# Kernel optimization log

Hardware: AMD Instinct MI355X
Metric: run time of the kernel (lower is better)

Reference implementation:

```python
import jax, jax.numpy as jnp
import numpy as np

N_NODES = 100000
N_EDGES = 3200000
N_FEAT = 64
HID = 64
GDIM = 32
N_CLASS = 2
NUM_GRAPHS = 16


def setup_inputs() -> dict:
    key = jax.random.key(0)
    ks = jax.random.split(key, 24)

    def w(k, fan_in, fan_out):
        return (jax.random.normal(k, (fan_in, fan_out), jnp.float32) / np.sqrt(fan_in)).astype(jnp.float32)

    inp = {
        'x': jax.random.normal(ks[0], (N_NODES, N_FEAT), jnp.float32),
        'edge_index': jax.random.randint(ks[1], (2, N_EDGES), 0, N_NODES, jnp.int32),
        'batch': jnp.sort(jax.random.randint(ks[2], (N_NODES,), 0, NUM_GRAPHS, jnp.int32)),
        # lin0: nr_features -> nhid0
        'lin0_w': w(ks[3], N_FEAT, HID), 'lin0_b': jnp.zeros((HID,), jnp.float32),
        # SAGEConv 1: lin_l (aggregated, with bias), lin_r (self, no bias)
        's1_lw': w(ks[4], HID, HID), 's1_lb': jnp.zeros((HID,), jnp.float32), 's1_rw': w(ks[5], HID, HID),
        # SAGEConv 2
        's2_lw': w(ks[6], HID, HID), 's2_lb': jnp.zeros((HID,), jnp.float32), 's2_rw': w(ks[7], HID, HID),
        # embedding heads
        'emb0_w': w(ks[8], HID, GDIM), 'emb0_b': jnp.zeros((GDIM,), jnp.float32),
        'emb1_w': w(ks[9], HID, GDIM), 'emb1_b': jnp.zeros((GDIM,), jnp.float32),
        'emb2_w': w(ks[10], HID, GDIM), 'emb2_b': jnp.zeros((GDIM,), jnp.float32),
        'merge_w': w(ks[11], 3 * GDIM, GDIM), 'merge_b': jnp.zeros((GDIM,), jnp.float32),
        # global attention pooling: gate_nn (GDIM->1), v_nn (GDIM->GDIM)
        'gate_w': w(ks[12], GDIM, 1), 'gate_b': jnp.zeros((1,), jnp.float32),
        'v_w': w(ks[13], GDIM, GDIM), 'v_b': jnp.zeros((GDIM,), jnp.float32),
        'out_w': w(ks[14], GDIM, N_CLASS), 'out_b': jnp.zeros((N_CLASS,), jnp.float32),
    }
    return inp


def _sage(x, src, dst, lw, lb, rw):
    # mean aggregation of source features at destination nodes
    deg = jax.ops.segment_sum(jnp.ones_like(src, jnp.float32), dst, num_segments=N_NODES)
    agg = jax.ops.segment_sum(x[src], dst, num_segments=N_NODES)
    mean = agg / jnp.maximum(deg, 1.0)[:, None]
    return mean @ lw + lb + x @ rw


def reference(x, edge_index, batch,
              lin0_w, lin0_b, s1_lw, s1_lb, s1_rw, s2_lw, s2_lb, s2_rw,
              emb0_w, emb0_b, emb1_w, emb1_b, emb2_w, emb2_b,
              merge_w, merge_b, gate_w, gate_b, v_w, v_b, out_w, out_b):
    src, dst = edge_index[0], edge_index[1]
    x0 = x @ lin0_w + lin0_b                       # [N, HID]
    x1 = _sage(x0, src, dst, s1_lw, s1_lb, s1_rw)  # [N, HID]
    x2 = _sage(x1, src, dst, s2_lw, s2_lb, s2_rw)  # [N, HID]
    # eval mode: dropout = identity
    e0 = jax.nn.relu(x0 @ emb0_w + emb0_b)
    e1 = jax.nn.relu(x1 @ emb1_w + emb1_b)
    e2 = jax.nn.relu(x2 @ emb2_w + emb2_b)
    xc = jax.nn.relu(jnp.concatenate([e0, e1, e2], axis=1) @ merge_w + merge_b)  # [N, GDIM]
    # global attention pooling with per-graph softmax
    g = (xc @ gate_w + gate_b)[:, 0]               # [N]
    v = xc @ v_w + v_b                             # [N, GDIM]
    m = jax.ops.segment_max(g, batch, num_segments=NUM_GRAPHS)
    e = jnp.exp(g - m[batch])
    d = jax.ops.segment_sum(e, batch, num_segments=NUM_GRAPHS)
    a = e / d[batch]
    pooled = jax.ops.segment_sum(a[:, None] * v, batch, num_segments=NUM_GRAPHS)  # [NG, GDIM]
    logits = pooled @ out_w + out_b                # [NG, 2]
    output1 = jax.nn.softmax(logits, axis=-1)
    output2 = logits
    return (output1, output2)
```

## Files before the change

### kernel.cpp

```cpp
#include <hip/hip_runtime.h>
#include <hip/hip_bf16.h>
#include <hip/hip_fp16.h>

#define N_NODES 100000
#define N_EDGES 3200000
#define HID 64
#define GDIM 32
#define NUM_GRAPHS 16
#define NB1 256
#define BSHIFT 9
#define B1 512

__device__ __forceinline__ unsigned fkey(float f) {
    unsigned u = __float_as_uint(f);
    return (u & 0x80000000u) ? ~u : (u | 0x80000000u);
}
__device__ __forceinline__ float funkey(unsigned k) {
    unsigned u = (k & 0x80000000u) ? (k ^ 0x80000000u) : ~k;
    return __uint_as_float(u);
}

struct half4 { __half2 lo, hi; };

__global__ __launch_bounds__(256) void hist1_kernel(const int* __restrict__ dst, int* __restrict__ h1, int E4) {
    __shared__ int h[NB1];
    int t = threadIdx.x, b = blockIdx.x;
    h[t] = 0;
    __syncthreads();
    for (int i = b * 256 + t; i < E4; i += B1 * 256) {
        int4 d = ((const int4*)dst)[i];
        atomicAdd(&h[d.x >> BSHIFT], 1);
        atomicAdd(&h[d.y >> BSHIFT], 1);
        atomicAdd(&h[d.z >> BSHIFT], 1);
        atomicAdd(&h[d.w >> BSHIFT], 1);
    }
    __syncthreads();
    h1[b * NB1 + t] = h[t];
}

__global__ __launch_bounds__(256) void scan1_kernel(const int* __restrict__ h1, int* __restrict__ off1,
                                                    int* __restrict__ bstart, int E) {
    __shared__ int ts[256];
    int t = threadIdx.x;
    int tot = 0;
    for (int k = 0; k < B1; k++) tot += h1[k * NB1 + t];
    ts[t] = tot;
    __syncthreads();
    for (int off = 1; off < 256; off <<= 1) {
        int v = (t >= off) ? ts[t - off] : 0;
        __syncthreads();
        ts[t] += v;
        __syncthreads();
    }
    int base = ts[t] - tot;
    bstart[t] = base;
    if (t == 255) bstart[256] = E;
    int run = base;
    for (int k = 0; k < B1; k++) { off1[k * NB1 + t] = run; run += h1[k * NB1 + t]; }
}

__global__ __launch_bounds__(256) void scatter1_kernel(const int* __restrict__ src, const int* __restrict__ dst,
                                                       const int* __restrict__ off1, int* __restrict__ pairs, int E4) {
    __shared__ int cur[NB1];
    int t = threadIdx.x, b = blockIdx.x;
    cur[t] = off1[b * NB1 + t];
    __syncthreads();
    for (int i = b * 256 + t; i < E4; i += B1 * 256) {
        int4 d = ((const int4*)dst)[i];
        int4 s = ((const int4*)src)[i];
        int p0 = atomicAdd(&cur[d.x >> BSHIFT], 1);
        int p1 = atomicAdd(&cur[d.y >> BSHIFT], 1);
        int p2 = atomicAdd(&cur[d.z >> BSHIFT], 1);
        int p3 = atomicAdd(&cur[d.w >> BSHIFT], 1);
        pairs[p0] = (s.x << BSHIFT) | (d.x & 511);
        pairs[p1] = (s.y << BSHIFT) | (d.y & 511);
        pairs[p2] = (s.z << BSHIFT) | (d.z & 511);
        pairs[p3] = (s.w << BSHIFT) | (d.w & 511);
    }
}

__global__ __launch_bounds__(256) void bucket_csr_kernel(const int* __restrict__ pairs, const int* __restrict__ bstart,
                                                         int* __restrict__ rowstart, int* __restrict__ csr,
                                                         int N, int E) {
    __shared__ int hist[512];
    __shared__ int ts[256];
    int b = blockIdx.x, t = threadIdx.x;
    int estart = bstart[b], eend = bstart[b + 1];
    hist[t] = 0; hist[t + 256] = 0;
    __syncthreads();
    for (int e = estart + t; e < eend; e += 256) {
        int pr = pairs[e];
        atomicAdd(&hist[pr & 511], 1);
    }
    __syncthreads();
    int a0 = hist[2 * t], a1 = hist[2 * t + 1];
    int s = a0 + a1;
    ts[t] = s;
    __syncthreads();
    for (int off = 1; off < 256; off <<= 1) {
        int v = (t >= off) ? ts[t - off] : 0;
        __syncthreads();
        ts[t] += v;
        __syncthreads();
    }
    int excl = ts[t] - s;
    __syncthreads();
    hist[2 * t]     = estart + excl;
    hist[2 * t + 1] = estart + excl + a0;
    int nb0 = b << BSHIFT;
    int i0 = nb0 + 2 * t, i1 = i0 + 1;
    if (i0 < N) rowstart[i0] = estart + excl;
    if (i1 < N) rowstart[i1] = estart + excl + a0;
    if (b == gridDim.x - 1 && t == 0) rowstart[N] = E;
    __syncthreads();
    for (int e = estart + t; e < eend; e += 256) {
        int pr = pairs[e];
        int p = atomicAdd(&hist[pr & 511], 1);
        csr[p] = pr >> BSHIFT;
    }
}

__global__ __launch_bounds__(256) void lin0_kernel(const float* __restrict__ x, const float* __restrict__ W,
                            const float* __restrict__ b, float* __restrict__ y, __half* __restrict__ yh, int N) {
    __shared__ __align__(16) float Wl[64 * 64];
    __shared__ float bl[64];
    int t = threadIdx.x;
    for (int i = t; i < 64 * 64; i += 256) Wl[i] = W[i];
    if (t < 64) bl[t] = b[t];
    __syncthreads();
    int row = blockIdx.x * 256 + t;
    if (row >= N) return;
    float acc[64];
#pragma unroll
    for (int j = 0; j < 64; j++) acc[j] = bl[j];
    const float4* xr = (const float4*)(x + (size_t)row * 64);
#pragma unroll
    for (int c = 0; c < 16; c++) {
        float4 xv = xr[c];
        float xs[4] = {xv.x, xv.y, xv.z, xv.w};
#pragma unroll
        for (int kk = 0; kk < 4; kk++) {
            int k = c * 4 + kk;
#pragma unroll
            for (int j4 = 0; j4 < 16; j4++) {
                float4 w = *(const float4*)&Wl[k * 64 + j4 * 4];
                acc[j4 * 4 + 0] += xs[kk] * w.x;
                acc[j4 * 4 + 1] += xs[kk] * w.y;
                acc[j4 * 4 + 2] += xs[kk] * w.z;
                acc[j4 * 4 + 3] += xs[kk] * w.w;
            }
        }
    }
    float4* yr = (float4*)(y + (size_t)row * 64);
#pragma unroll
    for (int c = 0; c < 16; c++)
        yr[c] = make_float4(acc[c * 4], acc[c * 4 + 1], acc[c * 4 + 2], acc[c * 4 + 3]);
    __half2* hr = (__half2*)(yh + (size_t)row * 64);
#pragma unroll
    for (int c = 0; c < 32; c++)
        hr[c] = __halves2half2(__float2half_rn(acc[c * 2]), __float2half_rn(acc[c * 2 + 1]));
}

__global__ __launch_bounds__(256) void agg_kernel(const __half* __restrict__ xh, const int* __restrict__ rowstart,
                           const int* __restrict__ csr, float* __restrict__ meanout, int N) {
    int wid = threadIdx.x >> 6, lane = threadIdx.x & 63;
    int node = blockIdx.x * 4 + wid;
    if (node >= N) return;
    int ro = rowstart[node], re = rowstart[node + 1];
    int g = lane >> 4, c4 = lane & 15;
    float4 acc = make_float4(0.f, 0.f, 0.f, 0.f);
    for (int base = ro; base < re; base += 64) {
        int rem = re - base;
        int idx = 0;
        if (lane < rem) idx = csr[base + lane];
        int kmax = rem < 64 ? rem : 64;
        for (int k = 0; k < kmax; k += 4) {
            int e = k + g;
            int s = __shfl(idx, e);
            if (e < kmax) {
                half4 hv = *(const half4*)(xh + (size_t)s * 64 + (c4 << 2));
                float2 f0 = __half22float2(hv.lo);
                float2 f1 = __half22float2(hv.hi);
                acc.x += f0.x; acc.y += f0.y; acc.z += f1.x; acc.w += f1.y;
            }
        }
    }
#pragma unroll
    for (int off = 16; off < 64; off <<= 1) {
        acc.x += __shfl_xor(acc.x, off);
        acc.y += __shfl_xor(acc.y, off);
        acc.z += __shfl_xor(acc.z, off);
        acc.w += __shfl_xor(acc.w, off);
    }
    int deg = re - ro;
    float inv = 1.0f / (float)(deg > 0 ? deg : 1);
    if (lane < 16) {
        ((float4*)(meanout + (size_t)node * 64))[c4] =
            make_float4(acc.x * inv, acc.y * inv, acc.z * inv, acc.w * inv);
    }
}

__global__ __launch_bounds__(256) void sage_kernel(const float* __restrict__ mean, const float* __restrict__ xin,
                            const float* __restrict__ lw, const float* __restrict__ lb,
                            const float* __restrict__ rw, float* __restrict__ xout,
                            __half* __restrict__ xhout, int N) {
    __shared__ __align__(16) float LW[64 * 64];
    __shared__ __align__(16) float RW[64 * 64];
    __shared__ float LB[64];
    int t = threadIdx.x;
    for (int i = t; i < 64 * 64; i += 256) { LW[i] = lw[i]; RW[i] = rw[i]; }
    if (t < 64) LB[t] = lb[t];
    __syncthreads();
    int row = blockIdx.x * 256 + t;
    if (row >= N) return;
    float acc[64];
#pragma unroll
    for (int j = 0; j < 64; j++) acc[j] = LB[j];
    const float4* mr = (const float4*)(mean + (size_t)row * 64);
    const float4* xr = (const float4*)(xin + (size_t)row * 64);
#pragma unroll
    for (int c = 0; c < 16; c++) {
        float4 xv = mr[c];
        float xs[4] = {xv.x, xv.y, xv.z, xv.w};
#pragma unroll
        for (int kk = 0; kk < 4; kk++) {
            int k = c * 4 + kk;
#pragma unroll
            for (int j4 = 0; j4 < 16; j4++) {
                float4 w = *(const float4*)&LW[k * 64 + j4 * 4];
                acc[j4 * 4 + 0] += xs[kk] * w.x;
                acc[j4 * 4 + 1] += xs[kk] * w.y;
                acc[j4 * 4 + 2] += xs[kk] * w.z;
                acc[j4 * 4 + 3] += xs[kk] * w.w;
            }
        }
    }
#pragma unroll
    for (int c = 0; c < 16; c++) {
        float4 xv = xr[c];
        float xs[4] = {xv.x, xv.y, xv.z, xv.w};
#pragma unroll
        for (int kk = 0; kk < 4; kk++) {
            int k = c * 4 + kk;
#pragma unroll
            for (int j4 = 0; j4 < 16; j4++) {
                float4 w = *(const float4*)&RW[k * 64 + j4 * 4];
                acc[j4 * 4 + 0] += xs[kk] * w.x;
                acc[j4 * 4 + 1] += xs[kk] * w.y;
                acc[j4 * 4 + 2] += xs[kk] * w.z;
                acc[j4 * 4 + 3] += xs[kk] * w.w;
            }
        }
    }
    float4* yr = (float4*)(xout + (size_t)row * 64);
#pragma unroll
    for (int c = 0; c < 16; c++)
        yr[c] = make_float4(acc[c * 4], acc[c * 4 + 1], acc[c * 4 + 2], acc[c * 4 + 3]);
    if (xhout) {
        __half2* hr = (__half2*)(xhout + (size_t)row * 64);
#pragma unroll
        for (int c = 0; c < 32; c++)
            hr[c] = __halves2half2(__float2half_rn(acc[c * 2]), __float2half_rn(acc[c * 2 + 1]));
    }
}

__global__ __launch_bounds__(256) void head_kernel(const float* __restrict__ x0, const float* __restrict__ x1,
                            const float* __restrict__ x2, const int* __restrict__ batch,
                            const float* __restrict__ e0w, const float* __restrict__ e0b,
                            const float* __restrict__ e1w, const float* __restrict__ e1b,
                            const float* __restrict__ e2w, const float* __restrict__ e2b,
                            const float* __restrict__ mw, const float* __restrict__ mb,
                            const float* __restrict__ gw, const float* __restrict__ gbp,
                            const float* __restrict__ vw, const float* __restrict__ vb,
                            float* __restrict__ gout, float* __restrict__ vout,
                            unsigned* __restrict__ mkey, int N) {
    __shared__ __align__(16) __half EW[3 * 2048];
    __shared__ __align__(16) __half MW[96 * 32];
    __shared__ __align__(16) __half VW[32 * 32];
    __shared__ float EB[96], MB[32], GW[32], VB[32];
    __shared__ float GB;
    __shared__ unsigned smax[16];
    int t = threadIdx.x;
    for (int i = t; i < 2048; i += 256) {
        EW[i]        = __float2half_rn(e0w[i]);
        EW[2048 + i] = __float2half_rn(e1w[i]);
        EW[4096 + i] = __float2half_rn(e2w[i]);
    }
    for (int i = t; i < 3072; i += 256) MW[i] = __float2half_rn(mw[i]);
    for (int i = t; i < 1024; i += 256) VW[i] = __float2half_rn(vw[i]);
    if (t < 32) { EB[t] = e0b[t]; EB[32 + t] = e1b[t]; EB[64 + t] = e2b[t];
                  MB[t] = mb[t]; GW[t] = gw[t]; VB[t] = vb[t]; }
    if (t == 0) GB = gbp[0];
    if (t < 16) smax[t] = 0u;
    __syncthreads();
    int node = blockIdx.x * 256 + t;
    if (node < N) {
        float xc[32];
#pragma unroll
        for (int j = 0; j < 32; j++) xc[j] = MB[j];
        const float* px[3] = {x0 + (size_t)node * 64, x1 + (size_t)node * 64, x2 + (size_t)node * 64};
        for (int h = 0; h < 3; h++) {
            float e[32];
#pragma unroll
            for (int j = 0; j < 32; j++) e[j] = EB[h * 32 + j];
            const float4* xr = (const float4*)px[h];
#pragma unroll
            for (int c = 0; c < 16; c++) {
                float4 xv = xr[c];
                float xs[4] = {xv.x, xv.y, xv.z, xv.w};
#pragma unroll
                for (int kk = 0; kk < 4; kk++) {
                    int k = c * 4 + kk;
#pragma unroll
                    for (int j4 = 0; j4 < 8; j4++) {
                        half4 hw = *(const half4*)&EW[h * 2048 + k * 32 + j4 * 4];
                        float2 w0 = __half22float2(hw.lo);
                        float2 w1 = __half22float2(hw.hi);
                        e[j4 * 4 + 0] += xs[kk] * w0.x;
                        e[j4 * 4 + 1] += xs[kk] * w0.y;
                        e[j4 * 4 + 2] += xs[kk] * w1.x;
                        e[j4 * 4 + 3] += xs[kk] * w1.y;
                    }
                }
            }
#pragma unroll
            for (int j = 0; j < 32; j++) e[j] = fmaxf(e[j], 0.f);
#pragma unroll
            for (int i = 0; i < 32; i++) {
#pragma unroll
                for (int j4 = 0; j4 < 8; j4++) {
                    half4 hw = *(const half4*)&MW[(h * 32 + i) * 32 + j4 * 4];
                    float2 w0 = __half22float2(hw.lo);
                    float2 w1 = __half22float2(hw.hi);
                    xc[j4 * 4 + 0] += e[i] * w0.x;
                    xc[j4 * 4 + 1] += e[i] * w0.y;
                    xc[j4 * 4 + 2] += e[i] * w1.x;
                    xc[j4 * 4 + 3] += e[i] * w1.y;
                }
            }
        }
#pragma unroll
        for (int j = 0; j < 32; j++) xc[j] = fmaxf(xc[j], 0.f);
        float g = GB;
#pragma unroll
        for (int i = 0; i < 32; i++) g += xc[i] * GW[i];
        float vv[32];
#pragma unroll
        for (int j = 0; j < 32; j++) vv[j] = VB[j];
#pragma unroll
        for (int i = 0; i < 32; i++) {
#pragma unroll
            for (int j4 = 0; j4 < 8; j4++) {
                half4 hw = *(const half4*)&VW[i * 32 + j4 * 4];
                float2 w0 = __half22float2(hw.lo);
                float2 w1 = __half22float2(hw.hi);
                vv[j4 * 4 + 0] += xc[i] * w0.x;
                vv[j4 * 4 + 1] += xc[i] * w0.y;
                vv[j4 * 4 + 2] += xc[i] * w1.x;
                vv[j4 * 4 + 3] += xc[i] * w1.y;
            }
        }
        gout[node] = g;
        float4* vr = (float4*)(vout + (size_t)node * 32);
#pragma unroll
        for (int c = 0; c < 8; c++)
            vr[c] = make_float4(vv[c * 4], vv[c * 4 + 1], vv[c * 4 + 2], vv[c * 4 + 3]);
        atomicMax(&smax[batch[node]], fkey(g));
    }
    __syncthreads();
    if (t < 16) atomicMax(&mkey[t], smax[t]);
}

__global__ __launch_bounds__(256) void pool_kernel(const float* __restrict__ g, const float* __restrict__ v,
                            const int* __restrict__ batch, const unsigned* __restrict__ mkey,
                            float* __restrict__ dsum, float* __restrict__ pooled, int N) {
    __shared__ float sd[16];
    __shared__ float sp[16 * 32];
    __shared__ float sm[16];
    int t = threadIdx.x;
    if (t < 16) { sd[t] = 0.f; sm[t] = funkey(mkey[t]); }
    for (int i = t; i < 512; i += 256) sp[i] = 0.f;
    __syncthreads();
    int node = blockIdx.x * 256 + t;
    if (node < N) {
        int b = batch[node];
        float e = __expf(g[node] - sm[b]);
        atomicAdd(&sd[b], e);
        const float4* vr = (const float4*)(v + (size_t)node * 32);
#pragma unroll
        for (int c = 0; c < 8; c++) {
            float4 vv = vr[c];
            atomicAdd(&sp[b * 32 + c * 4 + 0], e * vv.x);
            atomicAdd(&sp[b * 32 + c * 4 + 1], e * vv.y);
            atomicAdd(&sp[b * 32 + c * 4 + 2], e * vv.z);
            atomicAdd(&sp[b * 32 + c * 4 + 3], e * vv.w);
        }
    }
    __syncthreads();
    if (t < 16) atomicAdd(&dsum[t], sd[t]);
    for (int i = t; i < 512; i += 256) atomicAdd(&pooled[i], sp[i]);
}

__global__ __launch_bounds__(64) void final_kernel(const float* __restrict__ dsum, const float* __restrict__ pooled,
                             const float* __restrict__ ow, const float* __restrict__ ob,
                             float* __restrict__ out) {
    int t = threadIdx.x;
    if (t >= 16) return;
    float d = dsum[t];
    float l0 = ob[0], l1 = ob[1];
    for (int i = 0; i < 32; i++) {
        float p = pooled[t * 32 + i] / d;
        l0 += p * ow[i * 2 + 0];
        l1 += p * ow[i * 2 + 1];
    }
    float m = fmaxf(l0, l1);
    float e0 = __expf(l0 - m), e1 = __expf(l1 - m);
    float s = e0 + e1;
    out[t * 2 + 0] = e0 / s;
    out[t * 2 + 1] = e1 / s;
    out[32 + t * 2 + 0] = l0;
    out[32 + t * 2 + 1] = l1;
}

extern "C" void kernel_launch(void* const* d_in, const int* in_sizes, int n_in,
                              void* d_out, int out_size, void* d_ws, size_t ws_size,
                              hipStream_t stream) {
    const float* x       = (const float*)d_in[0];
    const int*   ei      = (const int*)d_in[1];
    const int*   batch   = (const int*)d_in[2];
    const float* lin0_w  = (const float*)d_in[3];
    const float* lin0_b  = (const float*)d_in[4];
    const float* s1_lw   = (const float*)d_in[5];
    const float* s1_lb   = (const float*)d_in[6];
    const float* s1_rw   = (const float*)d_in[7];
    const float* s2_lw   = (const float*)d_in[8];
    const float* s2_lb   = (const float*)d_in[9];
    const float* s2_rw   = (const float*)d_in[10];
    const float* e0w     = (const float*)d_in[11];
    const float* e0b     = (const float*)d_in[12];
    const float* e1w     = (const float*)d_in[13];
    const float* e1b     = (const float*)d_in[14];
    const float* e2w     = (const float*)d_in[15];
    const float* e2b     = (const float*)d_in[16];
    const float* mw      = (const float*)d_in[17];
    const float* mb      = (const float*)d_in[18];
    const float* gw      = (const float*)d_in[19];
    const float* gb      = (const float*)d_in[20];
    const float* vw      = (const float*)d_in[21];
    const float* vb      = (const float*)d_in[22];
    const float* ow      = (const float*)d_in[23];
    const float* ob      = (const float*)d_in[24];
    float* out = (float*)d_out;

    const int N = N_NODES, E = N_EDGES;
    const int* src = ei;
    const int* dst = ei + E;

    char* p = (char*)d_ws;
    auto carve = [&](size_t bytes) { char* r = p; p += (bytes + 255) & ~(size_t)255; return (void*)r; };
    float* x0      = (float*)carve((size_t)N * 64 * 4);
    float* x1      = (float*)carve((size_t)N * 64 * 4);
    float* x2      = (float*)carve((size_t)N * 64 * 4);
    __half* x0h    = (__half*)carve((size_t)N * 64 * 2);
    __half* x1h    = (__half*)carve((size_t)N * 64 * 2);
    float* meanb   = (float*)carve((size_t)N * 64 * 4);
    float* vbuf    = (float*)carve((size_t)N * 32 * 4);
    float* gbuf    = (float*)carve((size_t)N * 4);
    int*   csr     = (int*)carve((size_t)E * 4);
    int*   pairs   = (int*)carve((size_t)E * 4);
    int*   h1      = (int*)carve((size_t)B1 * NB1 * 4);
    int*   off1    = (int*)carve((size_t)B1 * NB1 * 4);
    int*   bstart  = (int*)carve((NB1 + 1) * 4);
    int*   rowstart= (int*)carve((size_t)(N + 1) * 4);
    unsigned* mkey = (unsigned*)carve(16 * 4);
    float* dsum    = (float*)carve(16 * 4);
    float* pooled  = (float*)carve(16 * 32 * 4);

    hipMemsetAsync(mkey, 0, 16 * 4, stream);
    hipMemsetAsync(dsum, 0, 16 * 4, stream);
    hipMemsetAsync(pooled, 0, 16 * 32 * 4, stream);

    const int E4 = E / 4;
    int nbl = (N + 255) / 256;
    int abl = (N + 3) / 4;
    const int NBUCK = (N + 511) >> BSHIFT;

    hist1_kernel<<<B1, 256, 0, stream>>>(dst, h1, E4);
    scan1_kernel<<<1, 256, 0, stream>>>(h1, off1, bstart, E);
    scatter1_kernel<<<B1, 256, 0, stream>>>(src, dst, off1, pairs, E4);
    bucket_csr_kernel<<<NBUCK, 256, 0, stream>>>(pairs, bstart, rowstart, csr, N, E);

    lin0_kernel<<<nbl, 256, 0, stream>>>(x, lin0_w, lin0_b, x0, x0h, N);

    agg_kernel<<<abl, 256, 0, stream>>>(x0h, rowstart, csr, meanb, N);
    sage_kernel<<<nbl, 256, 0, stream>>>(meanb, x0, s1_lw, s1_lb, s1_rw, x1, x1h, N);

    agg_kernel<<<abl, 256, 0, stream>>>(x1h, rowstart, csr, meanb, N);
    sage_kernel<<<nbl, 256, 0, stream>>>(meanb, x1, s2_lw, s2_lb, s2_rw, x2, (__half*)nullptr, N);

    head_kernel<<<nbl, 256, 0, stream>>>(x0, x1, x2, batch,
                                         e0w, e0b, e1w, e1b, e2w, e2b,
                                         mw, mb, gw, gb, vw, vb,
                                         gbuf, vbuf, mkey, N);

    pool_kernel<<<nbl, 256, 0, stream>>>(gbuf, vbuf, batch, mkey, dsum, pooled, N);

    final_kernel<<<1, 64, 0, stream>>>(dsum, pooled, ow, ob, out);
}
```

Baseline: 576.5 us.

## Split head kernel output columns across two threads per node with fp32 weights

The head kernel now assigns two threads per node, each computing half of the 32 output columns of the embedding, merge and value projections, and exchanges partial activations with cross-lane shuffles. Shared-memory weights are stored as fp32 instead of fp16, which removes per-use conversions and enables float4 loads. This halves per-thread register arrays and doubles the thread count, which should improve occupancy. The cost is that each node's input row is read twice, there is extra shuffle traffic, and the shared-memory footprint is larger.

```diff
diff --git a/kernel.cpp b/kernel.cpp
--- a/kernel.cpp
+++ b/kernel.cpp
@@ -274,35 +274,34 @@
                             const float* __restrict__ vw, const float* __restrict__ vb,
                             float* __restrict__ gout, float* __restrict__ vout,
                             unsigned* __restrict__ mkey, int N) {
-    __shared__ __align__(16) __half EW[3 * 2048];
-    __shared__ __align__(16) __half MW[96 * 32];
-    __shared__ __align__(16) __half VW[32 * 32];
+    __shared__ __align__(16) float EW[3 * 2048];
+    __shared__ __align__(16) float MW[96 * 32];
+    __shared__ __align__(16) float VW[32 * 32];
     __shared__ float EB[96], MB[32], GW[32], VB[32];
     __shared__ float GB;
     __shared__ unsigned smax[16];
     int t = threadIdx.x;
-    for (int i = t; i < 2048; i += 256) {
-        EW[i]        = __float2half_rn(e0w[i]);
-        EW[2048 + i] = __float2half_rn(e1w[i]);
-        EW[4096 + i] = __float2half_rn(e2w[i]);
-    }
-    for (int i = t; i < 3072; i += 256) MW[i] = __float2half_rn(mw[i]);
-    for (int i = t; i < 1024; i += 256) VW[i] = __float2half_rn(vw[i]);
+    for (int i = t; i < 2048; i += 256) { EW[i] = e0w[i]; EW[2048 + i] = e1w[i]; EW[4096 + i] = e2w[i]; }
+    for (int i = t; i < 3072; i += 256) MW[i] = mw[i];
+    for (int i = t; i < 1024; i += 256) VW[i] = vw[i];
     if (t < 32) { EB[t] = e0b[t]; EB[32 + t] = e1b[t]; EB[64 + t] = e2b[t];
                   MB[t] = mb[t]; GW[t] = gw[t]; VB[t] = vb[t]; }
     if (t == 0) GB = gbp[0];
     if (t < 16) smax[t] = 0u;
     __syncthreads();
-    int node = blockIdx.x * 256 + t;
+    int lane = t & 63, wid = t >> 6;
+    int half = lane >> 5, sub = lane & 31;
+    int node = blockIdx.x * 128 + wid * 32 + sub;
+    int cb = half * 16;
     if (node < N) {
-        float xc[32];
-#pragma unroll
-        for (int j = 0; j < 32; j++) xc[j] = MB[j];
+        float xc[16];
+#pragma unroll
+        for (int j = 0; j < 16; j++) xc[j] = MB[cb + j];
         const float* px[3] = {x0 + (size_t)node * 64, x1 + (size_t)node * 64, x2 + (size_t)node * 64};
         for (int h = 0; h < 3; h++) {
-            float e[32];
-#pragma unroll
-            for (int j = 0; j < 32; j++) e[j] = EB[h * 32 + j];
+            float e[16];
+#pragma unroll
+            for (int j = 0; j < 16; j++) e[j] = EB[h * 32 + cb + j];
             const float4* xr = (const float4*)px[h];
 #pragma unroll
             for (int c = 0; c < 16; c++) {
@@ -312,60 +311,69 @@
                 for (int kk = 0; kk < 4; kk++) {
                     int k = c * 4 + kk;
 #pragma unroll
-                    for (int j4 = 0; j4 < 8; j4++) {
-                        half4 hw = *(const half4*)&EW[h * 2048 + k * 32 + j4 * 4];
-                        float2 w0 = __half22float2(hw.lo);
-                        float2 w1 = __half22float2(hw.hi);
-                        e[j4 * 4 + 0] += xs[kk] * w0.x;
-                        e[j4 * 4 + 1] += xs[kk] * w0.y;
-                        e[j4 * 4 + 2] += xs[kk] * w1.x;
-                        e[j4 * 4 + 3] += xs[kk] * w1.y;
+                    for (int j4 = 0; j4 < 4; j4++) {
+                        float4 w = *(const float4*)&EW[h * 2048 + k * 32 + cb + j4 * 4];
+                        e[j4 * 4 + 0] += xs[kk] * w.x;
+                        e[j4 * 4 + 1] += xs[kk] * w.y;
+                        e[j4 * 4 + 2] += xs[kk] * w.z;
+                        e[j4 * 4 + 3] += xs[kk] * w.w;
                     }
                 }
             }
 #pragma unroll
-            for (int j = 0; j < 32; j++) e[j] = fmaxf(e[j], 0.f);
-#pragma unroll
-            for (int i = 0; i < 32; i++) {
-#pragma unroll
-                for (int j4 = 0; j4 < 8; j4++) {
-                    half4 hw = *(const half4*)&MW[(h * 32 + i) * 32 + j4 * 4];
-                    float2 w0 = __half22float2(hw.lo);
-                    float2 w1 = __half22float2(hw.hi);
-                    xc[j4 * 4 + 0] += e[i] * w0.x;
-                    xc[j4 * 4 + 1] += e[i] * w0.y;
-                    xc[j4 * 4 + 2] += e[i] * w1.x;
-                    xc[j4 * 4 + 3] += e[i] * w1.y;
+            for (int j = 0; j < 16; j++) e[j] = fmaxf(e[j], 0.f);
+            float eo[16];
+#pragma unroll
+            for (int j = 0; j < 16; j++) eo[j] = __shfl_xor(e[j], 32);
+#pragma unroll
+            for (int i = 0; i < 16; i++) {
+                float elo = (half == 0) ? e[i] : eo[i];
+                float ehi = (half == 0) ? eo[i] : e[i];
+#pragma unroll
+                for (int j4 = 0; j4 < 4; j4++) {
+                    float4 wl = *(const float4*)&MW[(h * 32 + i) * 32 + cb + j4 * 4];
+                    float4 wh = *(const float4*)&MW[(h * 32 + 16 + i) * 32 + cb + j4 * 4];
+                    xc[j4 * 4 + 0] += elo * wl.x + ehi * wh.x;
+                    xc[j4 * 4 + 1] += elo * wl.y + ehi * wh.y;
+                    xc[j4 * 4 + 2] += elo * wl.z + ehi * wh.z;
+                    xc[j4 * 4 + 3] += elo * wl.w + ehi * wh.w;
                 }
             }
         }
 #pragma unroll
-        for (int j = 0; j < 32; j++) xc[j] = fmaxf(xc[j], 0.f);
-        float g = GB;
-#pragma unroll
-        for (int i = 0; i < 32; i++) g += xc[i] * GW[i];
-        float vv[32];
-#pragma unroll
-        for (int j = 0; j < 32; j++) vv[j] = VB[j];
-#pragma unroll
-        for (int i = 0; i < 32; i++) {
-#pragma unroll
-            for (int j4 = 0; j4 < 8; j4++) {
-                half4 hw = *(const half4*)&VW[i * 32 + j4 * 4];
-                float2 w0 = __half22float2(hw.lo);
-                float2 w1 = __half22float2(hw.hi);
-                vv[j4 * 4 + 0] += xc[i] * w0.x;
-                vv[j4 * 4 + 1] += xc[i] * w0.y;
-                vv[j4 * 4 + 2] += xc[i] * w1.x;
-                vv[j4 * 4 + 3] += xc[i] * w1.y;
-            }
-        }
-        gout[node] = g;
-        float4* vr = (float4*)(vout + (size_t)node * 32);
-#pragma unroll
-        for (int c = 0; c < 8; c++)
+        for (int j = 0; j < 16; j++) xc[j] = fmaxf(xc[j], 0.f);
+        float gp = 0.f;
+#pragma unroll
+        for (int j = 0; j < 16; j++) gp += xc[j] * GW[cb + j];
+        float g = GB + gp + __shfl_xor(gp, 32);
+        float xo[16];
+#pragma unroll
+        for (int j = 0; j < 16; j++) xo[j] = __shfl_xor(xc[j], 32);
+        float vv[16];
+#pragma unroll
+        for (int j = 0; j < 16; j++) vv[j] = VB[cb + j];
+#pragma unroll
+        for (int i = 0; i < 16; i++) {
+            float xlo = (half == 0) ? xc[i] : xo[i];
+            float xhi = (half == 0) ? xo[i] : xc[i];
+#pragma unroll
+            for (int j4 = 0; j4 < 4; j4++) {
+                float4 wl = *(const float4*)&VW[i * 32 + cb + j4 * 4];
+                float4 wh = *(const float4*)&VW[(16 + i) * 32 + cb + j4 * 4];
+                vv[j4 * 4 + 0] += xlo * wl.x + xhi * wh.x;
+                vv[j4 * 4 + 1] += xlo * wl.y + xhi * wh.y;
+                vv[j4 * 4 + 2] += xlo * wl.z + xhi * wh.z;
+                vv[j4 * 4 + 3] += xlo * wl.w + xhi * wh.w;
+            }
+        }
+        float4* vr = (float4*)(vout + (size_t)node * 32 + cb);
+#pragma unroll
+        for (int c = 0; c < 4; c++)
             vr[c] = make_float4(vv[c * 4], vv[c * 4 + 1], vv[c * 4 + 2], vv[c * 4 + 3]);
-        atomicMax(&smax[batch[node]], fkey(g));
+        if (half == 0) {
+            gout[node] = g;
+            atomicMax(&smax[batch[node]], fkey(g));
+        }
     }
     __syncthreads();
     if (t < 16) atomicMax(&mkey[t], smax[t]);
@@ -483,6 +491,7 @@
     const int E4 = E / 4;
     int nbl = (N + 255) / 256;
     int abl = (N + 3) / 4;
+    int hbl = (N + 127) / 128;
     const int NBUCK = (N + 511) >> BSHIFT;
 
     hist1_kernel<<<B1, 256, 0, stream>>>(dst, h1, E4);
@@ -498,7 +507,7 @@
     agg_kernel<<<abl, 256, 0, stream>>>(x1h, rowstart, csr, meanb, N);
     sage_kernel<<<nbl, 256, 0, stream>>>(meanb, x1, s2_lw, s2_lb, s2_rw, x2, (__half*)nullptr, N);
 
-    head_kernel<<<nbl, 256, 0, stream>>>(x0, x1, x2, batch,
+    head_kernel<<<hbl, 256, 0, stream>>>(x0, x1, x2, batch,
                                          e0w, e0b, e1w, e1b, e2w, e2b,
                                          mw, mb, gw, gb, vw, vb,
                                          gbuf, vbuf, mkey, N);
```

Result: faster. 548.1 us (-4.9%).
